# Performance work log

Measured on AMD Instinct MI355X. Metric: run time of the kernel, lower is better.

The kernel has to match this reference:

```python
import jax, jax.numpy as jnp
import numpy as np

B, T, S1, S2 = 4, 256, 256, 256
D = 512          # tgt_dims == src_dims
V = 32000        # tgt_voc_size
H, DH = 8, 64    # heads, head_dims; HID = H*DH == D
HID = H * DH
VEXT = V + S1 + S2


def layer_norm(x):
    m = jnp.mean(x, axis=-1, keepdims=True)
    v = jnp.mean((x - m) ** 2, axis=-1, keepdims=True)
    return (x - m) / jnp.sqrt(v + 1e-5)


def copy_attention(query, key, qmask, kmask, Wq, bq, Wk, bk, Wv, bv, Wo, bo):
    # conv1d with kernel 1 == linear; weights are [out, in]
    b, t, _ = query.shape
    s = key.shape[1]
    q = (query @ Wq.T + bq).reshape(b, t, H, DH).transpose(0, 2, 1, 3) * (DH ** -0.5)
    k = (key @ Wk.T + bk).reshape(b, s, H, DH).transpose(0, 2, 1, 3)
    v = (key @ Wv.T + bv).reshape(b, s, H, DH).transpose(0, 2, 1, 3)
    att = jnp.einsum('bhtd,bhkd->bhtk', q, k)            # [B,H,T,S]
    out_att = att * kmask[:, None, None, :]              # multiplicative mask copy
    att = jnp.where((kmask == 0)[:, None, None, :], -jnp.inf, att)
    att = jax.nn.softmax(att, axis=-1)
    out = jnp.einsum('bhtk,bhkd->bhtd', att, v)
    out = out.transpose(0, 2, 1, 3).reshape(b, t, HID)
    out = (out @ Wo.T + bo) * qmask[:, :, None]
    out_att = out_att * qmask[:, None, :, None]
    return out_att.mean(axis=1), out                     # [B,T,S], [B,T,D]


def scatter_copy(att, map_idx):
    # copy_output[b, t, map_idx[b, s]] += att[b, t, s]  (accumulate=True)
    b, t, s = att.shape
    bi = jnp.arange(b)[:, None, None]
    ti = jnp.arange(t)[None, :, None]
    out = jnp.zeros((b, t, VEXT), att.dtype)
    return out.at[bi, ti, map_idx[:, None, :]].add(att)


def setup_inputs() -> dict:
    key = jax.random.key(0)
    ks = jax.random.split(key, 24)
    p = 0.02
    inp = {
        'tgt_dec_out': jax.random.normal(ks[0], (B, T, D), jnp.float32),
        'src1_key': jax.random.normal(ks[1], (B, S1, D), jnp.float32),
        'src1_map_idx': jax.random.randint(ks[2], (B, S1), 0, VEXT),
        'src2_key': jax.random.normal(ks[3], (B, S2, D), jnp.float32),
        'src2_map_idx': jax.random.randint(ks[4], (B, S2), 0, VEXT),
        'Wfc': jax.random.normal(ks[5], (V, D), jnp.float32) * p,
        'bfc': jnp.zeros((V,), jnp.float32),
        'Wp': jax.random.normal(ks[6], (3, 3 * D), jnp.float32) * p,
        'bp': jnp.zeros((3,), jnp.float32),
    }
    i = 7
    for a in ('1', '2'):
        for nm in ('Wq', 'Wk', 'Wv', 'Wo'):
            inp[nm + a] = jax.random.normal(ks[i], (HID, D), jnp.float32) * p
            inp[nm.replace('W', 'b') + a] = jnp.zeros((HID,), jnp.float32)
            i += 1
    return inp


def reference(tgt_dec_out, src1_key, src1_map_idx, src2_key, src2_map_idx,
              Wfc, bfc, Wp, bp,
              Wq1, bq1, Wk1, bk1, Wv1, bv1, Wo1, bo1,
              Wq2, bq2, Wk2, bk2, Wv2, bv2, Wo2, bo2):
    tgt_output = layer_norm(tgt_dec_out @ Wfc.T + bfc)          # [B,T,V]
    tgt_output = jnp.pad(tgt_output, ((0, 0), (0, 0), (0, S1 + S2)))  # [B,T,VEXT]
    tgt_mask = jnp.sign(jnp.abs(tgt_dec_out).sum(-1))
    src1_mask = jnp.sign(jnp.abs(src1_key).sum(-1))
    src2_mask = jnp.sign(jnp.abs(src2_key).sum(-1))
    att1, c1 = copy_attention(tgt_dec_out, src1_key, tgt_mask, src1_mask,
                              Wq1, bq1, Wk1, bk1, Wv1, bv1, Wo1, bo1)
    copy1 = scatter_copy(layer_norm(att1), src1_map_idx)
    att2, c2 = copy_attention(tgt_dec_out, src2_key, tgt_mask, src2_mask,
                              Wq2, bq2, Wk2, bk2, Wv2, bv2, Wo2, bo2)
    copy2 = scatter_copy(layer_norm(att2), src2_map_idx)
    p = jax.nn.softmax(jnp.concatenate([tgt_dec_out, c1, c2], axis=-1) @ Wp.T + bp, axis=-1)  # [B,T,3]
    out = tgt_output * p[..., 0:1] + copy1 * p[..., 1:2] + copy2 * p[..., 2:3]
    return out
```

## Files before the change

### kernel.cpp

```cpp
#include <hip/hip_runtime.h>
#include <hip/hip_bf16.h>
#include <cstdint>
#include <cstddef>

#define B_     4
#define T_     256
#define S_     256
#define D_     512
#define V_     32000
#define H_     8
#define DH_    64
#define HID_   512
#define VEXT_  32512
#define BT_    1024
#define CHUNK_ 8192
#define NSEG_  23

typedef __hip_bfloat16 bf16;
typedef __bf16 bf16x8 __attribute__((ext_vector_type(8)));
typedef float  f32x4  __attribute__((ext_vector_type(4)));

__device__ inline void store_val(float* p, float v) { *p = v; }
__device__ inline void store_val(bf16* p, float v)  { *p = __float2bfloat16(v); }

__device__ inline float bfbits2f(unsigned short u) {
    return __uint_as_float(((unsigned)u) << 16);
}
__device__ inline unsigned short f2bfbits(float f) {
    bf16 h = __float2bfloat16(f);
    union { bf16 h; unsigned short u; } cv; cv.h = h; return cv.u;
}

__global__ void probe_kernel(const unsigned short* __restrict__ x, int* __restrict__ flag,
                             float* __restrict__ rsum, float* __restrict__ rsq)
{
    __shared__ int cnt;
    if (threadIdx.x == 0) cnt = 0;
    __syncthreads();
    for (int i = threadIdx.x; i < BT_; i += 256) { rsum[i] = 0.f; rsq[i] = 0.f; }
    int c = 0;
    for (int i = threadIdx.x; i < 4096; i += 256) {
        const int e = (x[i] >> 7) & 0xFF;
        if (e >= 96 && e <= 159) c++;
    }
    atomicAdd(&cnt, c);
    __syncthreads();
    if (threadIdx.x == 0) *flag = (cnt < 3500) ? 1 : 0;
}

struct ConvArgs {
    const void* src[NSEG_];
    void*       dst[NSEG_];
};

__global__ __launch_bounds__(256)
void convert_all_kernel(ConvArgs a, const int* __restrict__ flag)
{
    const int CNT[NSEG_] = {
        524288, 524288, 524288, 32000, 4608, 3,
        262144, 262144, 512, 512,
        262144, 262144, 512, 512,
        262144, 262144, 512, 512,
        262144, 512, 262144, 512,
        16384000
    };
    const int fm = *flag;
    int seg = 0, blk = blockIdx.x;
    for (;;) {
        const int nb = (CNT[seg] + 8191) >> 13;
        if (blk < nb) break;
        blk -= nb; seg++;
    }
    const int n    = CNT[seg];
    const int j0   = blk << 13;
    const int jend = (n < j0 + 8192) ? n : (j0 + 8192);
    if (fm) {
        const float* s = (const float*)a.src[seg];
        unsigned short* d = (unsigned short*)a.dst[seg];
        for (int j = j0 + threadIdx.x * 4; j < jend; j += 1024) {
            if (j + 4 <= jend) {
                float4 v = *(const float4*)(s + j);
                ushort4 u;
                u.x = f2bfbits(v.x); u.y = f2bfbits(v.y);
                u.z = f2bfbits(v.z); u.w = f2bfbits(v.w);
                *(ushort4*)(d + j) = u;
            } else {
                for (int t = j; t < jend; t++) d[t] = f2bfbits(s[t]);
            }
        }
    } else {
        const unsigned short* s = (const unsigned short*)a.src[seg];
        unsigned short* d = (unsigned short*)a.dst[seg];
        for (int j = j0 + threadIdx.x * 4; j < jend; j += 1024) {
            if (j + 4 <= jend) {
                *(ushort4*)(d + j) = *(const ushort4*)(s + j);
            } else {
                for (int t = j; t < jend; t++) d[t] = s[t];
            }
        }
    }
}

__global__ void masks_kernel(const bf16* __restrict__ tgt, const bf16* __restrict__ s1,
                             const bf16* __restrict__ s2, float* __restrict__ mt,
                             float* __restrict__ m1, float* __restrict__ m2)
{
    const int row = blockIdx.x;
    const bf16* src; float* dst;
    if (row < BT_)           { src = tgt + (size_t)row * D_;            dst = mt + row; }
    else if (row < 2 * BT_)  { src = s1 + (size_t)(row - BT_) * D_;     dst = m1 + (row - BT_); }
    else                     { src = s2 + (size_t)(row - 2 * BT_) * D_; dst = m2 + (row - 2 * BT_); }
    const int lane = threadIdx.x;
    float s = 0.f;
    for (int i = lane; i < D_; i += 64) s += fabsf(__bfloat162float(src[i]));
#pragma unroll
    for (int off = 32; off; off >>= 1) s += __shfl_down(s, off);
    if (lane == 0) *dst = (s > 0.f) ? 1.f : 0.f;
}

template <typename OutT>
__device__ __forceinline__
void gemm_tile_body(const bf16* __restrict__ A, const bf16* __restrict__ Bw,
                    const bf16* __restrict__ bias, OutT* __restrict__ C,
                    const int K, const int ldC, const int m0, const int n0,
                    bf16* As, bf16* Bs)
{
    const int tid  = threadIdx.x;
    const int lane = tid & 63;
    const int wave = tid >> 6;
    const int quad = lane >> 4, l16 = lane & 15;
    const int wm = (wave >> 1) * 64, wn = (wave & 1) * 64;

    f32x4 acc[4][4];
#pragma unroll
    for (int i = 0; i < 4; i++)
#pragma unroll
        for (int j = 0; j < 4; j++) acc[i][j] = (f32x4){0.f, 0.f, 0.f, 0.f};

    const int row0 = tid >> 2;
    const int kp   = (tid & 3) * 8;
    const int sw   = (row0 & 3) << 3;
    const int swf  = (l16 & 3) << 3;

    for (int k0 = 0; k0 < K; k0 += 32) {
        uint4 a0 = *(const uint4*)(A  + (size_t)(m0 + row0)      * K + k0 + kp);
        uint4 a1 = *(const uint4*)(A  + (size_t)(m0 + row0 + 64) * K + k0 + kp);
        uint4 b0 = *(const uint4*)(Bw + (size_t)(n0 + row0)      * K + k0 + kp);
        uint4 b1 = *(const uint4*)(Bw + (size_t)(n0 + row0 + 64) * K + k0 + kp);
        __syncthreads();
        *(uint4*)(As + row0 * 32 + (kp ^ sw))        = a0;
        *(uint4*)(As + (row0 + 64) * 32 + (kp ^ sw)) = a1;
        *(uint4*)(Bs + row0 * 32 + (kp ^ sw))        = b0;
        *(uint4*)(Bs + (row0 + 64) * 32 + (kp ^ sw)) = b1;
        __syncthreads();

        bf16x8 af[4], bfv[4];
#pragma unroll
        for (int i = 0; i < 4; i++)
            af[i] = *(const bf16x8*)(As + (wm + i * 16 + l16) * 32 + ((quad * 8) ^ swf));
#pragma unroll
        for (int j = 0; j < 4; j++)
            bfv[j] = *(const bf16x8*)(Bs + (wn + j * 16 + l16) * 32 + ((quad * 8) ^ swf));
#pragma unroll
        for (int i = 0; i < 4; i++)
#pragma unroll
            for (int j = 0; j < 4; j++)
                acc[i][j] = __builtin_amdgcn_mfma_f32_16x16x32_bf16(af[i], bfv[j], acc[i][j], 0, 0, 0);
    }

#pragma unroll
    for (int i = 0; i < 4; i++)
#pragma unroll
        for (int j = 0; j < 4; j++) {
            const int nb = n0 + wn + j * 16 + l16;
            const float bv = __bfloat162float(bias[nb]);
#pragma unroll
            for (int r = 0; r < 4; r++) {
                const int m = m0 + wm + i * 16 + quad * 4 + r;
                store_val(C + (size_t)m * ldC + nb, acc[i][j][r] + bv);
            }
        }
}

struct Proj3Args {
    const bf16* A[3];
    const bf16* W[3];
    const bf16* b[3];
    bf16*       C[3];
};

__global__ __launch_bounds__(256)
void gemm_proj3_kernel(Proj3Args pa)
{
    __shared__ bf16 As[128 * 32];
    __shared__ bf16 Bs[128 * 32];
    const int z = blockIdx.z;
    gemm_tile_body<bf16>(pa.A[z], pa.W[z], pa.b[z], pa.C[z], D_, 1024,
                         blockIdx.y * 128, blockIdx.x * 128, As, Bs);
}

struct Out2Args {
    const bf16* A[2];
    const bf16* W[2];
    const bf16* b[2];
    float*      C[2];
};

__global__ __launch_bounds__(256)
void gemm_out2_kernel(Out2Args oa)
{
    __shared__ bf16 As[128 * 32];
    __shared__ bf16 Bs[128 * 32];
    const int z = blockIdx.z;
    gemm_tile_body<float>(oa.A[z], oa.W[z], oa.b[z], oa.C[z], D_, HID_,
                          blockIdx.y * 128, blockIdx.x * 128, As, Bs);
}

__global__ __launch_bounds__(256)
void gemm_fc_kernel(const bf16* __restrict__ A, const bf16* __restrict__ Bw,
                    const bf16* __restrict__ bias, void* __restrict__ Cv,
                    const int* __restrict__ flag,
                    float* __restrict__ rsum, float* __restrict__ rsq)
{
    __shared__ bf16 As[128 * 32];
    __shared__ bf16 Bs[128 * 32];
    const int fm = *flag;
    const int tid  = threadIdx.x;
    const int lane = tid & 63;
    const int wave = tid >> 6;
    const int quad = lane >> 4, l16 = lane & 15;
    const int f  = (blockIdx.x & 7) * 250 + (blockIdx.x >> 3);
    const int m0 = (f & 7) * 128;
    const int n0 = (f >> 3) * 128;
    const int wm = (wave >> 1) * 64, wn = (wave & 1) * 64;

    f32x4 acc[4][4];
#pragma unroll
    for (int i = 0; i < 4; i++)
#pragma unroll
        for (int j = 0; j < 4; j++) acc[i][j] = (f32x4){0.f, 0.f, 0.f, 0.f};

    const int row0 = tid >> 2;
    const int kp   = (tid & 3) * 8;
    const int sw   = (row0 & 3) << 3;
    const int swf  = (l16 & 3) << 3;

    for (int k0 = 0; k0 < D_; k0 += 32) {
        uint4 a0 = *(const uint4*)(A  + (size_t)(m0 + row0)      * D_ + k0 + kp);
        uint4 a1 = *(const uint4*)(A  + (size_t)(m0 + row0 + 64) * D_ + k0 + kp);
        uint4 b0 = *(const uint4*)(Bw + (size_t)(n0 + row0)      * D_ + k0 + kp);
        uint4 b1 = *(const uint4*)(Bw + (size_t)(n0 + row0 + 64) * D_ + k0 + kp);
        __syncthreads();
        *(uint4*)(As + row0 * 32 + (kp ^ sw))        = a0;
        *(uint4*)(As + (row0 + 64) * 32 + (kp ^ sw)) = a1;
        *(uint4*)(Bs + row0 * 32 + (kp ^ sw))        = b0;
        *(uint4*)(Bs + (row0 + 64) * 32 + (kp ^ sw)) = b1;
        __syncthreads();

        bf16x8 af[4], bfv[4];
#pragma unroll
        for (int i = 0; i < 4; i++)
            af[i] = *(const bf16x8*)(As + (wm + i * 16 + l16) * 32 + ((quad * 8) ^ swf));
#pragma unroll
        for (int j = 0; j < 4; j++)
            bfv[j] = *(const bf16x8*)(Bs + (wn + j * 16 + l16) * 32 + ((quad * 8) ^ swf));
#pragma unroll
        for (int i = 0; i < 4; i++)
#pragma unroll
            for (int j = 0; j < 4; j++)
                acc[i][j] = __builtin_amdgcn_mfma_f32_16x16x32_bf16(af[i], bfv[j], acc[i][j], 0, 0, 0);
    }

    float srow[4][4], sqr[4][4];
#pragma unroll
    for (int i = 0; i < 4; i++)
#pragma unroll
        for (int r = 0; r < 4; r++) { srow[i][r] = 0.f; sqr[i][r] = 0.f; }

#pragma unroll
    for (int i = 0; i < 4; i++)
#pragma unroll
        for (int j = 0; j < 4; j++) {
            const int nb = n0 + wn + j * 16 + l16;
            const float bv = __bfloat162float(bias[nb]);
#pragma unroll
            for (int r = 0; r < 4; r++) {
                const int m = m0 + wm + i * 16 + quad * 4 + r;
                const float val = acc[i][j][r] + bv;
                if (fm) ((float*)Cv)[(size_t)m * VEXT_ + nb] = val;
                else    ((bf16*)Cv)[(size_t)m * VEXT_ + nb] = __float2bfloat16(val);
                srow[i][r] += val;
                sqr[i][r]  += val * val;
            }
        }

#pragma unroll
    for (int i = 0; i < 4; i++)
#pragma unroll
        for (int r = 0; r < 4; r++) {
            float s = srow[i][r], q = sqr[i][r];
#pragma unroll
            for (int off = 1; off <= 8; off <<= 1) {
                s += __shfl_xor(s, off);
                q += __shfl_xor(q, off);
            }
            if (l16 == 0) {
                const int m = m0 + wm + i * 16 + quad * 4 + r;
                atomicAdd(&rsum[m], s);
                atomicAdd(&rsq[m],  q);
            }
        }
}

__global__ __launch_bounds__(256)
void fused_attn2_kernel(const bf16* __restrict__ qcat,
                        const bf16* __restrict__ kv1, const bf16* __restrict__ kv2,
                        const float* __restrict__ qmask,
                        const float* __restrict__ km1, const float* __restrict__ km2,
                        bf16* __restrict__ ctx1, bf16* __restrict__ ctx2,
                        float* __restrict__ lno1, float* __restrict__ lno2)
{
    __shared__ float qs[HID_];
    __shared__ float pvs[S_];
    __shared__ float part[4][DH_];
    __shared__ float red[4];
    const int y = blockIdx.y;
    const bf16* q  = qcat + y * HID_;
    const bf16* kv = y ? kv2 : kv1;
    const float* kmask = y ? km2 : km1;
    bf16* ctx = y ? ctx2 : ctx1;
    float* lnout = y ? lno2 : lno1;

    const int bt = blockIdx.x, b = bt >> 8, tid = threadIdx.x;
    const int lane = tid & 63, wv = tid >> 6;

    for (int d = tid; d < HID_; d += 256)
        qs[d] = __bfloat162float(q[(size_t)bt * 1024 + d]) * 0.125f;
    const float km = kmask[b * S_ + tid];
    const bool on = km != 0.f;
    __syncthreads();

    float msum = 0.f;
    for (int h = 0; h < H_; h++) {
        const bf16* kp = kv + (size_t)(b * S_ + tid) * 1024 + h * DH_;
        const float* qh = qs + h * DH_;
        float sc = 0.f;
#pragma unroll
        for (int d = 0; d < DH_; d += 8) {
            ushort4 u0 = *(const ushort4*)(kp + d);
            ushort4 u1 = *(const ushort4*)(kp + d + 4);
            sc += qh[d + 0] * bfbits2f(u0.x) + qh[d + 1] * bfbits2f(u0.y)
                + qh[d + 2] * bfbits2f(u0.z) + qh[d + 3] * bfbits2f(u0.w)
                + qh[d + 4] * bfbits2f(u1.x) + qh[d + 5] * bfbits2f(u1.y)
                + qh[d + 6] * bfbits2f(u1.z) + qh[d + 7] * bfbits2f(u1.w);
        }
        msum += sc;

        float x = on ? sc : -INFINITY;
        float m = x;
#pragma unroll
        for (int off = 32; off; off >>= 1) m = fmaxf(m, __shfl_down(m, off));
        __syncthreads();
        if (lane == 0) red[wv] = m;
        __syncthreads();
        const float mx = fmaxf(fmaxf(red[0], red[1]), fmaxf(red[2], red[3]));
        float e = (on && mx > -INFINITY) ? __expf(x - mx) : 0.f;
        float ts = e;
#pragma unroll
        for (int off = 32; off; off >>= 1) ts += __shfl_down(ts, off);
        __syncthreads();
        if (lane == 0) red[wv] = ts;
        __syncthreads();
        const float ssum = red[0] + red[1] + red[2] + red[3];
        const float inv = (ssum > 0.f) ? 1.f / ssum : 0.f;
        pvs[tid] = e * inv;
        __syncthreads();

        const bf16* vp = kv + (size_t)(b * S_ + wv * 64) * 1024 + 512 + h * DH_ + lane;
        float a = 0.f;
#pragma unroll 4
        for (int s = 0; s < 64; s++)
            a += pvs[wv * 64 + s] * __bfloat162float(vp[(size_t)s * 1024]);
        part[wv][lane] = a;
        __syncthreads();
        if (tid < 64) {
            float o = part[0][tid] + part[1][tid] + part[2][tid] + part[3][tid];
            ctx[(size_t)bt * HID_ + h * DH_ + tid] = __float2bfloat16(o);
        }
    }

    const float qm = qmask[bt];
    const float am = msum * (1.f / H_) * km * qm;
    float t1 = am;
#pragma unroll
    for (int off = 32; off; off >>= 1) t1 += __shfl_down(t1, off);
    __syncthreads();
    if (lane == 0) red[wv] = t1;
    __syncthreads();
    const float mean = (red[0] + red[1] + red[2] + red[3]) * (1.f / S_);
    float dv = (am - mean) * (am - mean);
#pragma unroll
    for (int off = 32; off; off >>= 1) dv += __shfl_down(dv, off);
    __syncthreads();
    if (lane == 0) red[wv] = dv;
    __syncthreads();
    const float rstd = rsqrtf(fmaxf((red[0] + red[1] + red[2] + red[3]) * (1.f / S_), 0.f) + 1e-5f);
    lnout[(size_t)bt * S_ + tid] = (am - mean) * rstd;
}

__global__ void pgate_kernel(const bf16* __restrict__ x, const float* __restrict__ c1,
                             const float* __restrict__ c2, const float* __restrict__ qmask,
                             const bf16* __restrict__ Wp, const bf16* __restrict__ bp,
                             float* __restrict__ p)
{
    const int bt = blockIdx.x;
    const int lane = threadIdx.x;
    const float qm = qmask[bt];
    float a0 = 0.f, a1 = 0.f, a2 = 0.f;
    for (int d = lane; d < D_; d += 64) {
        const float xv  = __bfloat162float(x[(size_t)bt * D_ + d]);
        const float c1v = c1[(size_t)bt * D_ + d] * qm;
        const float c2v = c2[(size_t)bt * D_ + d] * qm;
        a0 += xv * __bfloat162float(Wp[0 * 3 * D_ + d])
            + c1v * __bfloat162float(Wp[0 * 3 * D_ + D_ + d])
            + c2v * __bfloat162float(Wp[0 * 3 * D_ + 2 * D_ + d]);
        a1 += xv * __bfloat162float(Wp[1 * 3 * D_ + d])
            + c1v * __bfloat162float(Wp[1 * 3 * D_ + D_ + d])
            + c2v * __bfloat162float(Wp[1 * 3 * D_ + 2 * D_ + d]);
        a2 += xv * __bfloat162float(Wp[2 * 3 * D_ + d])
            + c1v * __bfloat162float(Wp[2 * 3 * D_ + D_ + d])
            + c2v * __bfloat162float(Wp[2 * 3 * D_ + 2 * D_ + d]);
    }
#pragma unroll
    for (int off = 32; off; off >>= 1) {
        a0 += __shfl_down(a0, off);
        a1 += __shfl_down(a1, off);
        a2 += __shfl_down(a2, off);
    }
    if (lane == 0) {
        float l0 = a0 + __bfloat162float(bp[0]);
        float l1 = a1 + __bfloat162float(bp[1]);
        float l2 = a2 + __bfloat162float(bp[2]);
        float mx = fmaxf(l0, fmaxf(l1, l2));
        float e0 = __expf(l0 - mx), e1 = __expf(l1 - mx), e2 = __expf(l2 - mx);
        float inv = 1.f / (e0 + e1 + e2);
        p[bt * 3 + 0] = e0 * inv; p[bt * 3 + 1] = e1 * inv; p[bt * 3 + 2] = e2 * inv;
    }
}

__global__ __launch_bounds__(256)
void final_kernel(void* __restrict__ outv, const int* __restrict__ flag,
                  const float* __restrict__ ln1, const float* __restrict__ ln2,
                  const int* __restrict__ map1, const int* __restrict__ map2,
                  const float* __restrict__ p,
                  const float* __restrict__ rsum, const float* __restrict__ rsq)
{
    __shared__ float chnk[CHUNK_];
    const int fm = *flag;
    const int bt = blockIdx.x, b = bt >> 8, tid = threadIdx.x;
    const float p0 = p[bt * 3], p1 = p[bt * 3 + 1], p2 = p[bt * 3 + 2];
    const float m = rsum[bt] * (1.f / V_);
    const float var = fmaxf(rsq[bt] * (1.f / V_) - m * m, 0.f);
    const float r = rsqrtf(var + 1e-5f);
    const size_t rbase = (size_t)bt * VEXT_;

    for (int c = 0; c < 4; c++) {
        const int jlo = c * CHUNK_;
        const int n = (VEXT_ - jlo < CHUNK_) ? (VEXT_ - jlo) : CHUNK_;
        for (int jj = tid * 4; jj < n; jj += 1024) {
            const int j = jlo + jj;
            float4 fv = {0.f, 0.f, 0.f, 0.f};
            if (j < V_) {
                float v0, v1, v2, v3;
                if (fm) {
                    float4 u = *(const float4*)((const float*)outv + rbase + j);
                    v0 = u.x; v1 = u.y; v2 = u.z; v3 = u.w;
                } else {
                    ushort4 u = *(const ushort4*)((const unsigned short*)outv + rbase + j);
                    v0 = bfbits2f(u.x); v1 = bfbits2f(u.y); v2 = bfbits2f(u.z); v3 = bfbits2f(u.w);
                }
                fv.x = p0 * (v0 - m) * r;
                fv.y = p0 * (v1 - m) * r;
                fv.z = p0 * (v2 - m) * r;
                fv.w = p0 * (v3 - m) * r;
            }
            *(float4*)(chnk + jj) = fv;
        }
        __syncthreads();
        for (int e = tid; e < 2 * S_; e += 256) {
            const int src = e >> 8, si = e & 255;
            const int j = (src ? map2 : map1)[b * S_ + si];
            if (j >= jlo && j < jlo + n) {
                const float val = (src ? p2 : p1) * (src ? ln2 : ln1)[(size_t)bt * S_ + si];
                atomicAdd(&chnk[j - jlo], val);
            }
        }
        __syncthreads();
        if (fm) {
            float* orow = (float*)outv + rbase;
            for (int jj = tid * 4; jj < n; jj += 1024)
                *(float4*)(orow + jlo + jj) = *(const float4*)(chnk + jj);
        } else {
            unsigned short* orow = (unsigned short*)outv + rbase;
            for (int jj = tid * 4; jj < n; jj += 1024) {
                float4 v = *(const float4*)(chnk + jj);
                ushort4 u;
                u.x = f2bfbits(v.x); u.y = f2bfbits(v.y); u.z = f2bfbits(v.z); u.w = f2bfbits(v.w);
                *(ushort4*)(orow + jlo + jj) = u;
            }
        }
        __syncthreads();
    }
}

extern "C" void kernel_launch(void* const* d_in, const int* in_sizes, int n_in,
                              void* d_out, int out_size, void* d_ws, size_t ws_size,
                              hipStream_t stream)
{
    const int* map1 = (const int*)d_in[2];
    const int* map2 = (const int*)d_in[4];

    char* w = (char*)d_ws;
    size_t off = 0;
    auto carve = [&](size_t bytes) -> char* {
        char* ptr = w + off;
        off = (off + bytes + 255) & ~(size_t)255;
        return ptr;
    };
    int* flag = (int*)carve(16);

    bf16* xc   = (bf16*)carve((size_t)BT_ * D_ * 2);
    bf16* s1c  = (bf16*)carve((size_t)B_ * S_ * D_ * 2);
    bf16* s2c  = (bf16*)carve((size_t)B_ * S_ * D_ * 2);
    bf16* Wfcc = (bf16*)carve((size_t)V_ * D_ * 2);
    bf16* bfcc = (bf16*)carve((size_t)V_ * 2);
    bf16* Wpc  = (bf16*)carve((size_t)3 * 3 * D_ * 2);
    bf16* bpc  = (bf16*)carve(3 * 2);
    bf16* Wqq  = (bf16*)carve((size_t)2 * HID_ * D_ * 2);
    bf16* bqq  = (bf16*)carve((size_t)2 * HID_ * 2);
    bf16* Wkv1 = (bf16*)carve((size_t)2 * HID_ * D_ * 2);
    bf16* bkv1 = (bf16*)carve((size_t)2 * HID_ * 2);
    bf16* Wkv2 = (bf16*)carve((size_t)2 * HID_ * D_ * 2);
    bf16* bkv2 = (bf16*)carve((size_t)2 * HID_ * 2);
    bf16* Wo1c = (bf16*)carve((size_t)HID_ * D_ * 2);
    bf16* bo1c = (bf16*)carve((size_t)HID_ * 2);
    bf16* Wo2c = (bf16*)carve((size_t)HID_ * D_ * 2);
    bf16* bo2c = (bf16*)carve((size_t)HID_ * 2);

    bf16*  qcat = (bf16*) carve((size_t)BT_ * 1024 * 2);
    bf16*  kv1  = (bf16*) carve((size_t)BT_ * 1024 * 2);
    bf16*  kv2  = (bf16*) carve((size_t)BT_ * 1024 * 2);
    bf16*  ctx1 = (bf16*) carve((size_t)BT_ * HID_ * 2);
    bf16*  ctx2 = (bf16*) carve((size_t)BT_ * HID_ * 2);
    float* c1   = (float*)carve((size_t)BT_ * HID_ * 4);
    float* c2   = (float*)carve((size_t)BT_ * HID_ * 4);
    float* ln1  = (float*)carve((size_t)BT_ * S_ * 4);
    float* ln2  = (float*)carve((size_t)BT_ * S_ * 4);
    float* p    = (float*)carve((size_t)BT_ * 3 * 4);
    float* mt   = (float*)carve((size_t)BT_ * 4);
    float* m1   = (float*)carve((size_t)BT_ * 4);
    float* m2   = (float*)carve((size_t)BT_ * 4);
    float* rsum = (float*)carve((size_t)BT_ * 4);
    float* rsq  = (float*)carve((size_t)BT_ * 4);
    (void)ws_size; (void)in_sizes; (void)n_in; (void)out_size;

    probe_kernel<<<1, 256, 0, stream>>>((const unsigned short*)d_in[0], flag, rsum, rsq);

    ConvArgs ca;
    ca.src[0]  = d_in[0];  ca.dst[0]  = xc;
    ca.src[1]  = d_in[1];  ca.dst[1]  = s1c;
    ca.src[2]  = d_in[3];  ca.dst[2]  = s2c;
    ca.src[3]  = d_in[6];  ca.dst[3]  = bfcc;
    ca.src[4]  = d_in[7];  ca.dst[4]  = Wpc;
    ca.src[5]  = d_in[8];  ca.dst[5]  = bpc;
    ca.src[6]  = d_in[9];  ca.dst[6]  = Wqq;
    ca.src[7]  = d_in[17]; ca.dst[7]  = Wqq + (size_t)HID_ * D_;
    ca.src[8]  = d_in[10]; ca.dst[8]  = bqq;
    ca.src[9]  = d_in[18]; ca.dst[9]  = bqq + HID_;
    ca.src[10] = d_in[11]; ca.dst[10] = Wkv1;
    ca.src[11] = d_in[13]; ca.dst[11] = Wkv1 + (size_t)HID_ * D_;
    ca.src[12] = d_in[12]; ca.dst[12] = bkv1;
    ca.src[13] = d_in[14]; ca.dst[13] = bkv1 + HID_;
    ca.src[14] = d_in[19]; ca.dst[14] = Wkv2;
    ca.src[15] = d_in[21]; ca.dst[15] = Wkv2 + (size_t)HID_ * D_;
    ca.src[16] = d_in[20]; ca.dst[16] = bkv2;
    ca.src[17] = d_in[22]; ca.dst[17] = bkv2 + HID_;
    ca.src[18] = d_in[15]; ca.dst[18] = Wo1c;
    ca.src[19] = d_in[16]; ca.dst[19] = bo1c;
    ca.src[20] = d_in[23]; ca.dst[20] = Wo2c;
    ca.src[21] = d_in[24]; ca.dst[21] = bo2c;
    ca.src[22] = d_in[5];  ca.dst[22] = Wfcc;
    convert_all_kernel<<<2462, 256, 0, stream>>>(ca, flag);

    masks_kernel<<<3 * BT_, 64, 0, stream>>>(xc, s1c, s2c, mt, m1, m2);

    gemm_fc_kernel<<<2000, 256, 0, stream>>>(xc, Wfcc, bfcc, d_out, flag, rsum, rsq);

    Proj3Args pa;
    pa.A[0] = xc;   pa.W[0] = Wqq;  pa.b[0] = bqq;  pa.C[0] = qcat;
    pa.A[1] = s1c;  pa.W[1] = Wkv1; pa.b[1] = bkv1; pa.C[1] = kv1;
    pa.A[2] = s2c;  pa.W[2] = Wkv2; pa.b[2] = bkv2; pa.C[2] = kv2;
    gemm_proj3_kernel<<<dim3(1024 / 128, BT_ / 128, 3), 256, 0, stream>>>(pa);

    fused_attn2_kernel<<<dim3(BT_, 2), 256, 0, stream>>>(qcat, kv1, kv2, mt, m1, m2,
                                                         ctx1, ctx2, ln1, ln2);

    Out2Args oa;
    oa.A[0] = ctx1; oa.W[0] = Wo1c; oa.b[0] = bo1c; oa.C[0] = c1;
    oa.A[1] = ctx2; oa.W[1] = Wo2c; oa.b[1] = bo2c; oa.C[1] = c2;
    gemm_out2_kernel<<<dim3(HID_ / 128, BT_ / 128, 2), 256, 0, stream>>>(oa);

    pgate_kernel<<<BT_, 64, 0, stream>>>(xc, c1, c2, mt, Wpc, bpc, p);

    final_kernel<<<BT_, 256, 0, stream>>>(d_out, flag, ln1, ln2, map1, map2, p, rsum, rsq);
}
```

Before: 524.5 us.

## Map one query row per wavefront in fused attention to drop block barriers

Restructures the fused attention kernel so each 64-lane wavefront handles one (b,t) query row, with each lane covering four key positions. All softmax and layernorm reductions become wave-level xor shuffles, which removes the many __syncthreads per head. The PV product is deferred until all heads' probabilities are stored in shared memory, then done once with 8-wide vector loads and vector stores. Per-thread register use and shared memory both rise, which may lower occupancy, and the key loads now use a strided per-lane access pattern.

```diff
diff --git a/kernel.cpp b/kernel.cpp
--- a/kernel.cpp
+++ b/kernel.cpp
@@ -320,92 +320,125 @@
                         bf16* __restrict__ ctx1, bf16* __restrict__ ctx2,
                         float* __restrict__ lno1, float* __restrict__ lno2)
 {
-    __shared__ float qs[HID_];
-    __shared__ float pvs[S_];
-    __shared__ float part[4][DH_];
-    __shared__ float red[4];
+    __shared__ float qs[4][HID_];
+    __shared__ float pvs[4][H_][260];
     const int y = blockIdx.y;
-    const bf16* q  = qcat + y * HID_;
+    const bf16* qb = qcat + y * HID_;
     const bf16* kv = y ? kv2 : kv1;
     const float* kmask = y ? km2 : km1;
     bf16* ctx = y ? ctx2 : ctx1;
     float* lnout = y ? lno2 : lno1;
 
-    const int bt = blockIdx.x, b = bt >> 8, tid = threadIdx.x;
+    const int tid = threadIdx.x;
     const int lane = tid & 63, wv = tid >> 6;
-
-    for (int d = tid; d < HID_; d += 256)
-        qs[d] = __bfloat162float(q[(size_t)bt * 1024 + d]) * 0.125f;
-    const float km = kmask[b * S_ + tid];
-    const bool on = km != 0.f;
-    __syncthreads();
-
-    float msum = 0.f;
+    const int bt = blockIdx.x * 4 + wv;
+    const int b  = bt >> 8;
+
+    {
+        const bf16* qp = qb + (size_t)bt * 1024 + lane * 8;
+        ushort4 u0 = *(const ushort4*)(qp);
+        ushort4 u1 = *(const ushort4*)(qp + 4);
+        float* qd = &qs[wv][lane * 8];
+        qd[0] = bfbits2f(u0.x) * 0.125f; qd[1] = bfbits2f(u0.y) * 0.125f;
+        qd[2] = bfbits2f(u0.z) * 0.125f; qd[3] = bfbits2f(u0.w) * 0.125f;
+        qd[4] = bfbits2f(u1.x) * 0.125f; qd[5] = bfbits2f(u1.y) * 0.125f;
+        qd[6] = bfbits2f(u1.z) * 0.125f; qd[7] = bfbits2f(u1.w) * 0.125f;
+    }
+
+    float kmv[4]; bool on[4];
+#pragma unroll
+    for (int i = 0; i < 4; i++) {
+        kmv[i] = kmask[b * S_ + lane + 64 * i];
+        on[i] = kmv[i] != 0.f;
+    }
+
+    const bf16* kbase = kv + (size_t)(b * S_ + lane) * 1024;
+    float msum[4] = {0.f, 0.f, 0.f, 0.f};
+
     for (int h = 0; h < H_; h++) {
-        const bf16* kp = kv + (size_t)(b * S_ + tid) * 1024 + h * DH_;
-        const float* qh = qs + h * DH_;
-        float sc = 0.f;
-#pragma unroll
-        for (int d = 0; d < DH_; d += 8) {
-            ushort4 u0 = *(const ushort4*)(kp + d);
-            ushort4 u1 = *(const ushort4*)(kp + d + 4);
-            sc += qh[d + 0] * bfbits2f(u0.x) + qh[d + 1] * bfbits2f(u0.y)
-                + qh[d + 2] * bfbits2f(u0.z) + qh[d + 3] * bfbits2f(u0.w)
-                + qh[d + 4] * bfbits2f(u1.x) + qh[d + 5] * bfbits2f(u1.y)
-                + qh[d + 6] * bfbits2f(u1.z) + qh[d + 7] * bfbits2f(u1.w);
-        }
-        msum += sc;
-
-        float x = on ? sc : -INFINITY;
-        float m = x;
-#pragma unroll
-        for (int off = 32; off; off >>= 1) m = fmaxf(m, __shfl_down(m, off));
-        __syncthreads();
-        if (lane == 0) red[wv] = m;
-        __syncthreads();
-        const float mx = fmaxf(fmaxf(red[0], red[1]), fmaxf(red[2], red[3]));
-        float e = (on && mx > -INFINITY) ? __expf(x - mx) : 0.f;
-        float ts = e;
-#pragma unroll
-        for (int off = 32; off; off >>= 1) ts += __shfl_down(ts, off);
-        __syncthreads();
-        if (lane == 0) red[wv] = ts;
-        __syncthreads();
-        const float ssum = red[0] + red[1] + red[2] + red[3];
-        const float inv = (ssum > 0.f) ? 1.f / ssum : 0.f;
-        pvs[tid] = e * inv;
-        __syncthreads();
-
-        const bf16* vp = kv + (size_t)(b * S_ + wv * 64) * 1024 + 512 + h * DH_ + lane;
-        float a = 0.f;
-#pragma unroll 4
-        for (int s = 0; s < 64; s++)
-            a += pvs[wv * 64 + s] * __bfloat162float(vp[(size_t)s * 1024]);
-        part[wv][lane] = a;
-        __syncthreads();
-        if (tid < 64) {
-            float o = part[0][tid] + part[1][tid] + part[2][tid] + part[3][tid];
-            ctx[(size_t)bt * HID_ + h * DH_ + tid] = __float2bfloat16(o);
-        }
+        const float* qh = &qs[wv][h * DH_];
+        float sc[4] = {0.f, 0.f, 0.f, 0.f};
+#pragma unroll
+        for (int d0 = 0; d0 < DH_; d0 += 8) {
+            const float qv0 = qh[d0 + 0], qv1 = qh[d0 + 1], qv2 = qh[d0 + 2], qv3 = qh[d0 + 3];
+            const float qv4 = qh[d0 + 4], qv5 = qh[d0 + 5], qv6 = qh[d0 + 6], qv7 = qh[d0 + 7];
+#pragma unroll
+            for (int i = 0; i < 4; i++) {
+                const bf16* kp = kbase + (size_t)i * 64 * 1024 + h * DH_ + d0;
+                ushort4 u0 = *(const ushort4*)(kp);
+                ushort4 u1 = *(const ushort4*)(kp + 4);
+                sc[i] += qv0 * bfbits2f(u0.x) + qv1 * bfbits2f(u0.y)
+                       + qv2 * bfbits2f(u0.z) + qv3 * bfbits2f(u0.w)
+                       + qv4 * bfbits2f(u1.x) + qv5 * bfbits2f(u1.y)
+                       + qv6 * bfbits2f(u1.z) + qv7 * bfbits2f(u1.w);
+            }
+        }
+        float xs[4];
+        float mx = -INFINITY;
+#pragma unroll
+        for (int i = 0; i < 4; i++) {
+            msum[i] += sc[i];
+            xs[i] = on[i] ? sc[i] : -INFINITY;
+            mx = fmaxf(mx, xs[i]);
+        }
+#pragma unroll
+        for (int off = 32; off; off >>= 1) mx = fmaxf(mx, __shfl_xor(mx, off));
+        float e[4], ts = 0.f;
+        const bool live = (mx > -INFINITY);
+#pragma unroll
+        for (int i = 0; i < 4; i++) {
+            e[i] = (on[i] && live) ? __expf(xs[i] - mx) : 0.f;
+            ts += e[i];
+        }
+#pragma unroll
+        for (int off = 32; off; off >>= 1) ts += __shfl_xor(ts, off);
+        const float inv = (ts > 0.f) ? 1.f / ts : 0.f;
+#pragma unroll
+        for (int i = 0; i < 4; i++)
+            pvs[wv][h][lane + 64 * i] = e[i] * inv;
+    }
+
+    {
+        const float* prow = pvs[wv][lane >> 3];
+        const bf16* vp = kv + (size_t)(b * S_) * 1024 + 512 + lane * 8;
+        float o0 = 0.f, o1 = 0.f, o2 = 0.f, o3 = 0.f, o4 = 0.f, o5 = 0.f, o6 = 0.f, o7 = 0.f;
+#pragma unroll 8
+        for (int s = 0; s < S_; s++) {
+            ushort4 u0 = *(const ushort4*)(vp + (size_t)s * 1024);
+            ushort4 u1 = *(const ushort4*)(vp + (size_t)s * 1024 + 4);
+            const float pv = prow[s];
+            o0 += pv * bfbits2f(u0.x); o1 += pv * bfbits2f(u0.y);
+            o2 += pv * bfbits2f(u0.z); o3 += pv * bfbits2f(u0.w);
+            o4 += pv * bfbits2f(u1.x); o5 += pv * bfbits2f(u1.y);
+            o6 += pv * bfbits2f(u1.z); o7 += pv * bfbits2f(u1.w);
+        }
+        ushort4 w0, w1;
+        w0.x = f2bfbits(o0); w0.y = f2bfbits(o1); w0.z = f2bfbits(o2); w0.w = f2bfbits(o3);
+        w1.x = f2bfbits(o4); w1.y = f2bfbits(o5); w1.z = f2bfbits(o6); w1.w = f2bfbits(o7);
+        bf16* cp = ctx + (size_t)bt * HID_ + lane * 8;
+        *(ushort4*)(cp) = w0;
+        *(ushort4*)(cp + 4) = w1;
     }
 
     const float qm = qmask[bt];
-    const float am = msum * (1.f / H_) * km * qm;
-    float t1 = am;
-#pragma unroll
-    for (int off = 32; off; off >>= 1) t1 += __shfl_down(t1, off);
-    __syncthreads();
-    if (lane == 0) red[wv] = t1;
-    __syncthreads();
-    const float mean = (red[0] + red[1] + red[2] + red[3]) * (1.f / S_);
-    float dv = (am - mean) * (am - mean);
-#pragma unroll
-    for (int off = 32; off; off >>= 1) dv += __shfl_down(dv, off);
-    __syncthreads();
-    if (lane == 0) red[wv] = dv;
-    __syncthreads();
-    const float rstd = rsqrtf(fmaxf((red[0] + red[1] + red[2] + red[3]) * (1.f / S_), 0.f) + 1e-5f);
-    lnout[(size_t)bt * S_ + tid] = (am - mean) * rstd;
+    float am[4], s1 = 0.f;
+#pragma unroll
+    for (int i = 0; i < 4; i++) {
+        am[i] = msum[i] * (1.f / H_) * kmv[i] * qm;
+        s1 += am[i];
+    }
+#pragma unroll
+    for (int off = 32; off; off >>= 1) s1 += __shfl_xor(s1, off);
+    const float mean = s1 * (1.f / S_);
+    float dv = 0.f;
+#pragma unroll
+    for (int i = 0; i < 4; i++) dv += (am[i] - mean) * (am[i] - mean);
+#pragma unroll
+    for (int off = 32; off; off >>= 1) dv += __shfl_xor(dv, off);
+    const float rstd = rsqrtf(fmaxf(dv * (1.f / S_), 0.f) + 1e-5f);
+#pragma unroll
+    for (int i = 0; i < 4; i++)
+        lnout[(size_t)bt * S_ + lane + 64 * i] = (am[i] - mean) * rstd;
 }
 
 __global__ void pgate_kernel(const bf16* __restrict__ x, const float* __restrict__ c1,
@@ -602,8 +635,8 @@
     pa.A[2] = s2c;  pa.W[2] = Wkv2; pa.b[2] = bkv2; pa.C[2] = kv2;
     gemm_proj3_kernel<<<dim3(1024 / 128, BT_ / 128, 3), 256, 0, stream>>>(pa);
 
-    fused_attn2_kernel<<<dim3(BT_, 2), 256, 0, stream>>>(qcat, kv1, kv2, mt, m1, m2,
-                                                         ctx1, ctx2, ln1, ln2);
+    fused_attn2_kernel<<<dim3(BT_ / 4, 2), 256, 0, stream>>>(qcat, kv1, kv2, mt, m1, m2,
+                                                             ctx1, ctx2, ln1, ln2);
 
     Out2Args oa;
     oa.A[0] = ctx1; oa.W[0] = Wo1c; oa.b[0] = bo1c; oa.C[0] = c1;
```

Result: faster. 496.9 us (-5.3%).
